# Kernel tuning notes

Hardware: AMD Instinct MI355X
Metric: run time of the kernel (lower is better)

The kernel has to match this reference:

```python
import jax, jax.numpy as jnp
import numpy as np

B, S, D = 4, 2048, 1024
H, DK, DV = 16, 64, 64


def setup_inputs() -> dict:
    key = jax.random.key(0)
    ks = jax.random.split(key, 8)
    Q = jax.random.normal(ks[0], (B, S, D), dtype=jnp.float32)
    K = jax.random.normal(ks[1], (B, S, D), dtype=jnp.float32)
    V = jax.random.normal(ks[2], (B, S, D), dtype=jnp.float32)
    attn_mask = jax.random.randint(ks[3], (B, S, S), 0, 2).astype(jnp.bool_)
    sc = 1.0 / np.sqrt(D)
    W_Q = jax.random.normal(ks[4], (D, H * DK), dtype=jnp.float32) * sc
    W_K = jax.random.normal(ks[5], (D, H * DK), dtype=jnp.float32) * sc
    W_V = jax.random.normal(ks[6], (D, H * DV), dtype=jnp.float32) * sc
    W_O = jax.random.normal(ks[7], (H * DV, D), dtype=jnp.float32) * sc
    return {"Q": Q, "K": K, "V": V, "attn_mask": attn_mask,
            "W_Q": W_Q, "W_K": W_K, "W_V": W_V, "W_O": W_O}


def reference(Q, K, V, attn_mask, W_Q, W_K, W_V, W_O):
    b = Q.shape[0]
    # project and split heads: [b, h, s, d]
    q = (Q @ W_Q).reshape(b, -1, H, DK).transpose(0, 2, 1, 3)
    k = (K @ W_K).reshape(b, -1, H, DK).transpose(0, 2, 1, 3)
    v = (V @ W_V).reshape(b, -1, H, DV).transpose(0, 2, 1, 3)
    scale = 1.0 / jnp.sqrt(jnp.asarray(DK, dtype=q.dtype))
    scores = jnp.einsum('bhsd,bhtd->bhst', q, k) * scale  # [b,h,s,s]
    scores = jnp.where(attn_mask[:, None, :, :], jnp.asarray(-1e9, dtype=scores.dtype), scores)
    attn = jax.nn.softmax(scores, axis=-1)
    ctx = jnp.einsum('bhst,bhtd->bhsd', attn, v)  # [b,h,s,dv]
    ctx = ctx.transpose(0, 2, 1, 3).reshape(b, -1, H * DV)
    return ctx @ W_O
```

## Files before the change

### kernel.cpp

```cpp
#include <hip/hip_runtime.h>
#include <stdint.h>


typedef float f32x4 __attribute__((ext_vector_type(4)));
typedef float f32x16 __attribute__((ext_vector_type(16)));
typedef __bf16 bf16x8 __attribute__((ext_vector_type(8)));
typedef int i32x2 __attribute__((ext_vector_type(2)));

__device__ __forceinline__ unsigned short f2b(float f) {
  union { float f; uint32_t u; } v; v.f = f;
  return (unsigned short)((v.u + 0x7FFFu + ((v.u >> 16) & 1u)) >> 16);
}

__device__ __forceinline__ uint32_t pkbf(float a, float b) {
  union { __bf16 h[2]; uint32_t u; } c;
  c.h[0] = (__bf16)a; c.h[1] = (__bf16)b;
  return c.u;
}

__device__ __forceinline__ float fast_exp2(float x) {
#if __has_builtin(__builtin_amdgcn_exp2f)
  return __builtin_amdgcn_exp2f(x);
#else
  return exp2f(x);
#endif
}

__device__ __forceinline__ f32x4 mfma16(bf16x8 a, bf16x8 b, f32x4 c) {
  return __builtin_amdgcn_mfma_f32_16x16x32_bf16(a, b, c, 0, 0, 0);
}

__device__ __forceinline__ f32x16 mfma32(bf16x8 a, bf16x8 b, f32x16 c) {
  return __builtin_amdgcn_mfma_f32_32x32x16_bf16(a, b, c, 0, 0, 0);
}

__device__ __forceinline__ void gld_lds16(const void* g, void* l) {
  typedef __attribute__((address_space(1))) const uint32_t GU;
  typedef __attribute__((address_space(3))) uint32_t LU;
  __builtin_amdgcn_global_load_lds((GU*)g, (LU*)l, 16, 0, 0);
}

__global__ __launch_bounds__(256) void prep_w_kernel(
    const float* __restrict__ w0, const float* __restrict__ w1,
    const float* __restrict__ w2, const float* __restrict__ w3,
    unsigned short* __restrict__ wt) {
  __shared__ float tile[64][68];
  const float* w = (blockIdx.z == 0) ? w0 : (blockIdx.z == 1) ? w1
                  : (blockIdx.z == 2) ? w2 : w3;
  unsigned short* out = wt + (size_t)blockIdx.z * (1024u * 1024u);
  const int t = threadIdx.x;
  {
    const int kr = t >> 2, cc = (t & 3) << 4;
    const float* src = w + (size_t)(blockIdx.y * 64 + kr) * 1024 + blockIdx.x * 64 + cc;
#pragma unroll
    for (int i = 0; i < 4; ++i)
      *(float4*)&tile[kr][cc + i * 4] = ((const float4*)src)[i];
  }
  __syncthreads();
  const int cl = t >> 2, kc = (t & 3) << 4;
  const int c = blockIdx.x * 64 + cl;
  union { unsigned short u[8]; uint4 q; } p0, p1;
#pragma unroll
  for (int j = 0; j < 8; ++j) {
    p0.u[j] = f2b(tile[kc + j][cl]);
    p1.u[j] = f2b(tile[kc + 8 + j][cl]);
  }
  char* rowp = (char*)out + (size_t)c * 2048;
  const uint32_t sw = (uint32_t)(c & 7) << 4;
  const uint32_t b0 = (uint32_t)(blockIdx.y * 64 + kc) * 2;
  *(uint4*)(rowp + (b0 ^ sw)) = p0.q;
  *(uint4*)(rowp + ((b0 + 16) ^ sw)) = p1.q;
}

__global__ __launch_bounds__(256) void mask_pack_kernel(
    const void* __restrict__ mask, uint32_t* __restrict__ bits) {
  __shared__ int flag;
  if (threadIdx.x == 0) flag = 0;
  __syncthreads();
  if (threadIdx.x < 64) {
    uchar4 cb = ((const uchar4*)mask)[threadIdx.x];
    if ((cb.y | cb.z | cb.w) != 0) atomicOr(&flag, 1);
  }
  __syncthreads();
  const bool is32 = (flag == 0);
  const int* ip = (const int*)mask;
  const unsigned char* bp = (const unsigned char*)mask;
  const int gw = (blockIdx.x * 256 + threadIdx.x) >> 6;
  const int lane = threadIdx.x & 63;
  const size_t base = (size_t)gw * 8192;
  for (int it = 0; it < 128; ++it) {
    size_t idx = base + (size_t)it * 64 + lane;
    int v = is32 ? ip[idx] : (int)bp[idx];
    unsigned long long m = __ballot(v != 0);
    if (lane == 0) bits[idx >> 5] = (uint32_t)m;
    if (lane == 32) bits[idx >> 5] = (uint32_t)(m >> 32);
  }
}

template <int AMODE, int OMODE>
__global__ __launch_bounds__(256) void gemm_kernel(
    const void* __restrict__ Asrc, const unsigned short* __restrict__ BT,
    void* __restrict__ Out) {
  __shared__ __align__(16) char As[128 * 128];
  __shared__ __align__(16) char Bs[128 * 128];
  const int tid = threadIdx.x;
  const int lane = tid & 63, wave = tid >> 6;
  const int g = lane >> 4, l15 = lane & 15;
  const int wm = wave >> 1, wn = wave & 1;
  const int mbase = blockIdx.x * 128, nbase = blockIdx.y * 128;

  f32x4 acc[4][4];
  const f32x4 fz = {0.f, 0.f, 0.f, 0.f};
#pragma unroll
  for (int i = 0; i < 4; ++i)
#pragma unroll
    for (int j = 0; j < 4; ++j) acc[i][j] = fz;

  for (int kb = 0; kb < 16; ++kb) {
    if (AMODE == 0) {
#pragma unroll
      for (int rr = 0; rr < 4; ++rr) {
        int row = rr * 32 + (tid >> 3);
        int kc = (tid & 7) * 8;
        const float* ap = (const float*)Asrc + (size_t)(mbase + row) * 1024 + kb * 64 + kc;
        float4 a0 = ((const float4*)ap)[0];
        float4 a1 = ((const float4*)ap)[1];
        union { __bf16 h[8]; uint4 q; } pk;
        pk.h[0] = (__bf16)a0.x; pk.h[1] = (__bf16)a0.y;
        pk.h[2] = (__bf16)a0.z; pk.h[3] = (__bf16)a0.w;
        pk.h[4] = (__bf16)a1.x; pk.h[5] = (__bf16)a1.y;
        pk.h[6] = (__bf16)a1.z; pk.h[7] = (__bf16)a1.w;
        *(uint4*)(As + row * 128 + ((kc * 2) ^ ((row & 7) << 4))) = pk.q;
      }
    } else {
      const char* ag = (const char*)Asrc + (size_t)mbase * 2048 + (size_t)kb * 128;
#pragma unroll
      for (int c = 0; c < 4; ++c) {
        int ch = wave * 4 + c;
        int row = ch * 8 + (lane >> 3);
        gld_lds16(ag + (size_t)row * 2048 + (lane & 7) * 16, As + ch * 1024);
      }
    }
    {
      const char* bg = (const char*)BT + (size_t)nbase * 2048 + (size_t)kb * 128;
#pragma unroll
      for (int c = 0; c < 4; ++c) {
        int ch = wave * 4 + c;
        int row = ch * 8 + (lane >> 3);
        gld_lds16(bg + (size_t)row * 2048 + (lane & 7) * 16, Bs + ch * 1024);
      }
    }
    __syncthreads();
#pragma unroll
    for (int kk = 0; kk < 2; ++kk) {
      bf16x8 af[4], bf[4];
#pragma unroll
      for (int mf = 0; mf < 4; ++mf) {
        int row = wm * 64 + mf * 16 + l15;
        af[mf] = *(const bf16x8*)(As + row * 128 + (((kk * 32 + g * 8) * 2) ^ ((row & 7) << 4)));
      }
#pragma unroll
      for (int nf = 0; nf < 4; ++nf) {
        int row = wn * 64 + nf * 16 + l15;
        bf[nf] = *(const bf16x8*)(Bs + row * 128 + (((kk * 32 + g * 8) * 2) ^ ((row & 7) << 4)));
      }
#pragma unroll
      for (int mf = 0; mf < 4; ++mf)
#pragma unroll
        for (int nf = 0; nf < 4; ++nf)
          acc[mf][nf] = mfma16(af[mf], bf[nf], acc[mf][nf]);
    }
    __syncthreads();
  }

  const int colbase = nbase + wn * 64 + l15;
#pragma unroll
  for (int mf = 0; mf < 4; ++mf) {
    const int grow0 = mbase + wm * 64 + mf * 16 + g * 4;
    if (OMODE == 3) {
      float* op = (float*)Out;
#pragma unroll
      for (int r = 0; r < 4; ++r)
#pragma unroll
        for (int nf = 0; nf < 4; ++nf)
          op[(size_t)(grow0 + r) * 1024 + colbase + nf * 16] = acc[mf][nf][r];
    } else if (OMODE == 0) {
      unsigned short* op = (unsigned short*)Out;
#pragma unroll
      for (int r = 0; r < 4; ++r) {
        int grow = grow0 + r, bq = grow >> 11, s = grow & 2047;
#pragma unroll
        for (int nf = 0; nf < 4; ++nf) {
          int col = colbase + nf * 16, hh = col >> 6, d = col & 63;
          op[((size_t)(bq * 16 + hh) * 2048 + s) * 64 + d] = f2b(acc[mf][nf][r]);
        }
      }
    } else if (OMODE == 1) {
      char* op = (char*)Out;
#pragma unroll
      for (int r = 0; r < 4; ++r) {
        int grow = grow0 + r, bq = grow >> 11, s = grow & 2047;
#pragma unroll
        for (int nf = 0; nf < 4; ++nf) {
          int col = colbase + nf * 16, hh = col >> 6, d = col & 63;
          *(unsigned short*)(op + ((size_t)(bq * 16 + hh) * 2048 + s) * 128 +
                             ((d * 2) ^ ((s & 7) << 4))) = f2b(acc[mf][nf][r]);
        }
      }
    } else {
      char* op = (char*)Out;
      const int bq = grow0 >> 11, s0 = grow0 & 2047;
#pragma unroll
      for (int nf = 0; nf < 4; ++nf) {
        int col = colbase + nf * 16, hh = col >> 6, d = col & 63;
        union { unsigned short u[4]; uint2 q; } pk;
#pragma unroll
        for (int r = 0; r < 4; ++r) pk.u[r] = f2b(acc[mf][nf][r]);
        *(uint2*)(op + ((size_t)(bq * 16 + hh) * 64 + d) * 4096 +
                  ((s0 * 2) ^ ((d & 7) << 4))) = pk.q;
      }
    }
  }
}

__global__ __launch_bounds__(256, 2) void attn_kernel(
    const unsigned short* __restrict__ q_ws, const char* __restrict__ k_ws,
    const char* __restrict__ vt_ws, const uint32_t* __restrict__ bits,
    char* __restrict__ ctx) {
  __shared__ __align__(16) char ks[2][8192];
  __shared__ __align__(16) char vs[2][8192];
  const int tid = threadIdx.x;
  const int lane = tid & 63, wave = tid >> 6;
  const int hi = lane >> 5, l31 = lane & 31;
  const int qt = blockIdx.x, h = blockIdx.y, b = blockIdx.z;
  const int bh = b * 16 + h;
  const int qw = qt * 128 + wave * 32;
  const char* kg = k_ws + (size_t)bh * (2048 * 128);
  const char* vg = vt_ws + (size_t)bh * (64 * 4096);

  bf16x8 bq[4];
  {
    const unsigned short* qp = q_ws + ((size_t)bh * 2048 + qw + l31) * 64 + hi * 8;
#pragma unroll
    for (int c = 0; c < 4; ++c) bq[c] = *(const bf16x8*)(qp + c * 16);
  }
  const uint32_t* mrow = bits + ((size_t)b * 2048 + qw + l31) * 64;
  uint2 mk = *(const uint2*)(mrow);

  const f32x16 fz16 = {0.f, 0.f, 0.f, 0.f, 0.f, 0.f, 0.f, 0.f,
                       0.f, 0.f, 0.f, 0.f, 0.f, 0.f, 0.f, 0.f};
  f32x16 oacc0 = fz16, oacc1 = fz16;
  float lsum = 0.f;

  const float C1 = 0.18033688011112042f;
  const float C2 = -17.312340490667562f;
  const uint32_t swl = (uint32_t)(l31 & 7) << 4;

  auto stage = [&](int t, int buf) {
    const char* kb = kg + (size_t)t * 8192;
#pragma unroll
    for (int rr = 0; rr < 2; ++rr) {
      int ch = wave * 2 + rr;
      gld_lds16(kb + ch * 1024 + lane * 16, ks[buf] + ch * 1024);
    }
    const char* vb = vg + (size_t)t * 128;
#pragma unroll
    for (int rr = 0; rr < 2; ++rr) {
      int ch = wave * 2 + rr;
      int dv = ch * 8 + (lane >> 3);
      gld_lds16(vb + (size_t)dv * 4096 + (lane & 7) * 16, vs[buf] + ch * 1024);
    }
  };

  stage(0, 0);
  __syncthreads();

  for (int tt = 0; tt < 32; ++tt) {
    const int cur = tt & 1;
    uint2 mnext = mk;
    if (tt < 31) {
      stage(tt + 1, cur ^ 1);
      mnext = *(const uint2*)(mrow + (tt + 1) * 2);
    }
    const char* kbuf = ks[cur];
    f32x16 s0 = fz16, s1 = fz16;
    __builtin_amdgcn_s_setprio(1);
#pragma unroll
    for (int c = 0; c < 4; ++c) {
      bf16x8 a0 = *(const bf16x8*)(kbuf + l31 * 128 + ((c * 32 + hi * 16) ^ swl));
      bf16x8 a1 = *(const bf16x8*)(kbuf + (32 + l31) * 128 + ((c * 32 + hi * 16) ^ swl));
      s0 = mfma32(a0, bq[c], s0);
      s1 = mfma32(a1, bq[c], s1);
    }
    __builtin_amdgcn_s_setprio(0);

    bf16x8 pa[4];
#pragma unroll
    for (int T = 0; T < 2; ++T) {
      const f32x16 sv = (T == 0) ? s0 : s1;
      const uint32_t wh = ((T == 0) ? mk.x : mk.y) >> (hi * 4);
      float e[16];
#pragma unroll
      for (int r = 0; r < 16; ++r) {
        float ex = fast_exp2(fmaf(sv[r], C1, C2));
        e[r] = ((wh >> ((r & 3) + 8 * (r >> 2))) & 1u) ? 0.f : ex;
        lsum += e[r];
      }
#pragma unroll
      for (int c2 = 0; c2 < 2; ++c2) {
        const int rb = c2 * 8;
        uint32_t x = pkbf(e[rb + 0], e[rb + 1]);
        uint32_t y = pkbf(e[rb + 2], e[rb + 3]);
        uint32_t z = pkbf(e[rb + 4], e[rb + 5]);
        uint32_t w2 = pkbf(e[rb + 6], e[rb + 7]);
        i32x2 sxz = __builtin_amdgcn_permlane32_swap((int)x, (int)z, false, false);
        i32x2 syw = __builtin_amdgcn_permlane32_swap((int)y, (int)w2, false, false);
        union { uint32_t u[4]; bf16x8 v; } fa;
        fa.u[0] = (uint32_t)sxz[0]; fa.u[1] = (uint32_t)syw[0];
        fa.u[2] = (uint32_t)sxz[1]; fa.u[3] = (uint32_t)syw[1];
        pa[T * 2 + c2] = fa.v;
      }
    }

    const char* vbuf = vs[cur];
    __builtin_amdgcn_s_setprio(1);
#pragma unroll
    for (int kc = 0; kc < 4; ++kc) {
      bf16x8 b0 = *(const bf16x8*)(vbuf + l31 * 128 + ((kc * 32 + hi * 16) ^ swl));
      bf16x8 b1 = *(const bf16x8*)(vbuf + (32 + l31) * 128 + ((kc * 32 + hi * 16) ^ swl));
      oacc0 = mfma32(pa[kc], b0, oacc0);
      oacc1 = mfma32(pa[kc], b1, oacc1);
    }
    __builtin_amdgcn_s_setprio(0);
    __syncthreads();
    mk = mnext;
  }

  lsum += __shfl_xor(lsum, 32);
  const float linv = 1.f / lsum;
  const int col0 = h * 64 + l31, col1 = col0 + 32;
#pragma unroll
  for (int r = 0; r < 16; ++r) {
    const int qloc = (r & 3) + 8 * (r >> 2) + 4 * hi;
    const float li = __shfl(linv, qloc);
    const int srow = b * 2048 + qw + qloc;
    const uint32_t swr = (uint32_t)(srow & 7) << 4;
    *(unsigned short*)(ctx + (size_t)srow * 2048 + ((col0 * 2) ^ swr)) = f2b(oacc0[r] * li);
    *(unsigned short*)(ctx + (size_t)srow * 2048 + ((col1 * 2) ^ swr)) = f2b(oacc1[r] * li);
  }
}

extern "C" void kernel_launch(void* const* d_in, const int* in_sizes, int n_in,
                              void* d_out, int out_size, void* d_ws, size_t ws_size,
                              hipStream_t stream) {
  (void)in_sizes; (void)n_in; (void)out_size; (void)ws_size;
  const float* Q = (const float*)d_in[0];
  const float* K = (const float*)d_in[1];
  const float* V = (const float*)d_in[2];
  const void* mask = d_in[3];
  const float* WQ = (const float*)d_in[4];
  const float* WK = (const float*)d_in[5];
  const float* WV = (const float*)d_in[6];
  const float* WO = (const float*)d_in[7];

  char* ws = (char*)d_ws;
  unsigned short* wt = (unsigned short*)ws;
  unsigned short* q_ws = (unsigned short*)(ws + (8ll << 20));
  char* k_ws = ws + (24ll << 20);
  char* vt_ws = ws + (40ll << 20);
  char* ctx = ws + (56ll << 20);
  uint32_t* bits = (uint32_t*)(ws + (72ll << 20));

  prep_w_kernel<<<dim3(16, 16, 4), 256, 0, stream>>>(WQ, WK, WV, WO, wt);
  mask_pack_kernel<<<dim3(512), 256, 0, stream>>>(mask, bits);
  gemm_kernel<0, 0><<<dim3(64, 8), 256, 0, stream>>>((const void*)Q, wt, (void*)q_ws);
  gemm_kernel<0, 1><<<dim3(64, 8), 256, 0, stream>>>((const void*)K, wt + (1u << 20), (void*)k_ws);
  gemm_kernel<0, 2><<<dim3(64, 8), 256, 0, stream>>>((const void*)V, wt + (2u << 20), (void*)vt_ws);
  attn_kernel<<<dim3(16, 16, 4), 256, 0, stream>>>(q_ws, k_ws, vt_ws, bits, ctx);
  gemm_kernel<1, 3><<<dim3(64, 8), 256, 0, stream>>>((const void*)ctx, wt + (3u << 20), d_out);
}
```

Baseline: 474.2 us.

## Batch QKV projections into one launch and compute softmax row sums via MFMA

Result: no change. 476.6 us (+0.5%).

```diff
diff --git a/kernel.cpp b/kernel.cpp
--- a/kernel.cpp
+++ b/kernel.cpp
@@ -97,12 +97,16 @@
   }
 }
 
-template <int AMODE, int OMODE>
-__global__ __launch_bounds__(256) void gemm_kernel(
-    const void* __restrict__ Asrc, const unsigned short* __restrict__ BT,
-    void* __restrict__ Out) {
+__global__ __launch_bounds__(256, 3) void proj_gemm_kernel(
+    const float* __restrict__ Qin, const float* __restrict__ Kin,
+    const float* __restrict__ Vin, const unsigned short* __restrict__ wt,
+    unsigned short* __restrict__ q_ws, char* __restrict__ k_ws,
+    char* __restrict__ vt_ws) {
   __shared__ __align__(16) char As[128 * 128];
   __shared__ __align__(16) char Bs[128 * 128];
+  const int z = blockIdx.z;
+  const float* Asrc = (z == 0) ? Qin : (z == 1) ? Kin : Vin;
+  const unsigned short* BT = wt + (size_t)z * (1u << 20);
   const int tid = threadIdx.x;
   const int lane = tid & 63, wave = tid >> 6;
   const int g = lane >> 4, l15 = lane & 15;
@@ -117,12 +121,12 @@
     for (int j = 0; j < 4; ++j) acc[i][j] = fz;
 
   for (int kb = 0; kb < 16; ++kb) {
-    if (AMODE == 0) {
+    {
 #pragma unroll
       for (int rr = 0; rr < 4; ++rr) {
         int row = rr * 32 + (tid >> 3);
         int kc = (tid & 7) * 8;
-        const float* ap = (const float*)Asrc + (size_t)(mbase + row) * 1024 + kb * 64 + kc;
+        const float* ap = Asrc + (size_t)(mbase + row) * 1024 + kb * 64 + kc;
         float4 a0 = ((const float4*)ap)[0];
         float4 a1 = ((const float4*)ap)[1];
         union { __bf16 h[8]; uint4 q; } pk;
@@ -132,14 +136,6 @@
         pk.h[6] = (__bf16)a1.z; pk.h[7] = (__bf16)a1.w;
         *(uint4*)(As + row * 128 + ((kc * 2) ^ ((row & 7) << 4))) = pk.q;
       }
-    } else {
-      const char* ag = (const char*)Asrc + (size_t)mbase * 2048 + (size_t)kb * 128;
-#pragma unroll
-      for (int c = 0; c < 4; ++c) {
-        int ch = wave * 4 + c;
-        int row = ch * 8 + (lane >> 3);
-        gld_lds16(ag + (size_t)row * 2048 + (lane & 7) * 16, As + ch * 1024);
-      }
     }
     {
       const char* bg = (const char*)BT + (size_t)nbase * 2048 + (size_t)kb * 128;
@@ -177,15 +173,8 @@
 #pragma unroll
   for (int mf = 0; mf < 4; ++mf) {
     const int grow0 = mbase + wm * 64 + mf * 16 + g * 4;
-    if (OMODE == 3) {
-      float* op = (float*)Out;
-#pragma unroll
-      for (int r = 0; r < 4; ++r)
-#pragma unroll
-        for (int nf = 0; nf < 4; ++nf)
-          op[(size_t)(grow0 + r) * 1024 + colbase + nf * 16] = acc[mf][nf][r];
-    } else if (OMODE == 0) {
-      unsigned short* op = (unsigned short*)Out;
+    if (z == 0) {
+      unsigned short* op = q_ws;
 #pragma unroll
       for (int r = 0; r < 4; ++r) {
         int grow = grow0 + r, bq = grow >> 11, s = grow & 2047;
@@ -195,8 +184,8 @@
           op[((size_t)(bq * 16 + hh) * 2048 + s) * 64 + d] = f2b(acc[mf][nf][r]);
         }
       }
-    } else if (OMODE == 1) {
-      char* op = (char*)Out;
+    } else if (z == 1) {
+      char* op = k_ws;
 #pragma unroll
       for (int r = 0; r < 4; ++r) {
         int grow = grow0 + r, bq = grow >> 11, s = grow & 2047;
@@ -208,7 +197,7 @@
         }
       }
     } else {
-      char* op = (char*)Out;
+      char* op = vt_ws;
       const int bq = grow0 >> 11, s0 = grow0 & 2047;
 #pragma unroll
       for (int nf = 0; nf < 4; ++nf) {
@@ -223,7 +212,79 @@
   }
 }
 
-__global__ __launch_bounds__(256, 2) void attn_kernel(
+__global__ __launch_bounds__(256) void out_gemm_kernel(
+    const char* __restrict__ Asrc, const unsigned short* __restrict__ BT,
+    float* __restrict__ Out) {
+  __shared__ __align__(16) char As[128 * 128];
+  __shared__ __align__(16) char Bs[128 * 128];
+  const int tid = threadIdx.x;
+  const int lane = tid & 63, wave = tid >> 6;
+  const int g = lane >> 4, l15 = lane & 15;
+  const int wm = wave >> 1, wn = wave & 1;
+  const int mbase = blockIdx.x * 128, nbase = blockIdx.y * 128;
+
+  f32x4 acc[4][4];
+  const f32x4 fz = {0.f, 0.f, 0.f, 0.f};
+#pragma unroll
+  for (int i = 0; i < 4; ++i)
+#pragma unroll
+    for (int j = 0; j < 4; ++j) acc[i][j] = fz;
+
+  for (int kb = 0; kb < 16; ++kb) {
+    {
+      const char* ag = Asrc + (size_t)mbase * 2048 + (size_t)kb * 128;
+#pragma unroll
+      for (int c = 0; c < 4; ++c) {
+        int ch = wave * 4 + c;
+        int row = ch * 8 + (lane >> 3);
+        gld_lds16(ag + (size_t)row * 2048 + (lane & 7) * 16, As + ch * 1024);
+      }
+    }
+    {
+      const char* bg = (const char*)BT + (size_t)nbase * 2048 + (size_t)kb * 128;
+#pragma unroll
+      for (int c = 0; c < 4; ++c) {
+        int ch = wave * 4 + c;
+        int row = ch * 8 + (lane >> 3);
+        gld_lds16(bg + (size_t)row * 2048 + (lane & 7) * 16, Bs + ch * 1024);
+      }
+    }
+    __syncthreads();
+#pragma unroll
+    for (int kk = 0; kk < 2; ++kk) {
+      bf16x8 af[4], bf[4];
+#pragma unroll
+      for (int mf = 0; mf < 4; ++mf) {
+        int row = wm * 64 + mf * 16 + l15;
+        af[mf] = *(const bf16x8*)(As + row * 128 + (((kk * 32 + g * 8) * 2) ^ ((row & 7) << 4)));
+      }
+#pragma unroll
+      for (int nf = 0; nf < 4; ++nf) {
+        int row = wn * 64 + nf * 16 + l15;
+        bf[nf] = *(const bf16x8*)(Bs + row * 128 + (((kk * 32 + g * 8) * 2) ^ ((row & 7) << 4)));
+      }
+#pragma unroll
+      for (int mf = 0; mf < 4; ++mf)
+#pragma unroll
+        for (int nf = 0; nf < 4; ++nf)
+          acc[mf][nf] = mfma16(af[mf], bf[nf], acc[mf][nf]);
+    }
+    __syncthreads();
+  }
+
+  const int colbase = nbase + wn * 64 + l15;
+#pragma unroll
+  for (int mf = 0; mf < 4; ++mf) {
+    const int grow0 = mbase + wm * 64 + mf * 16 + g * 4;
+#pragma unroll
+    for (int r = 0; r < 4; ++r)
+#pragma unroll
+      for (int nf = 0; nf < 4; ++nf)
+        Out[(size_t)(grow0 + r) * 1024 + colbase + nf * 16] = acc[mf][nf][r];
+  }
+}
+
+__global__ __launch_bounds__(256, 4) void attn_kernel(
     const unsigned short* __restrict__ q_ws, const char* __restrict__ k_ws,
     const char* __restrict__ vt_ws, const uint32_t* __restrict__ bits,
     char* __restrict__ ctx) {
@@ -249,8 +310,12 @@
 
   const f32x16 fz16 = {0.f, 0.f, 0.f, 0.f, 0.f, 0.f, 0.f, 0.f,
                        0.f, 0.f, 0.f, 0.f, 0.f, 0.f, 0.f, 0.f};
-  f32x16 oacc0 = fz16, oacc1 = fz16;
-  float lsum = 0.f;
+  f32x16 oacc0 = fz16, oacc1 = fz16, sacc = fz16;
+
+  union { unsigned short u[8]; bf16x8 v; } onesu;
+#pragma unroll
+  for (int i = 0; i < 8; ++i) onesu.u[i] = 0x3F80;
+  const bf16x8 ones = onesu.v;
 
   const float C1 = 0.18033688011112042f;
   const float C2 = -17.312340490667562f;
@@ -304,7 +369,6 @@
       for (int r = 0; r < 16; ++r) {
         float ex = fast_exp2(fmaf(sv[r], C1, C2));
         e[r] = ((wh >> ((r & 3) + 8 * (r >> 2))) & 1u) ? 0.f : ex;
-        lsum += e[r];
       }
 #pragma unroll
       for (int c2 = 0; c2 < 2; ++c2) {
@@ -330,19 +394,18 @@
       bf16x8 b1 = *(const bf16x8*)(vbuf + (32 + l31) * 128 + ((kc * 32 + hi * 16) ^ swl));
       oacc0 = mfma32(pa[kc], b0, oacc0);
       oacc1 = mfma32(pa[kc], b1, oacc1);
+      sacc = mfma32(pa[kc], ones, sacc);
     }
     __builtin_amdgcn_s_setprio(0);
     __syncthreads();
     mk = mnext;
   }
 
-  lsum += __shfl_xor(lsum, 32);
-  const float linv = 1.f / lsum;
   const int col0 = h * 64 + l31, col1 = col0 + 32;
 #pragma unroll
   for (int r = 0; r < 16; ++r) {
     const int qloc = (r & 3) + 8 * (r >> 2) + 4 * hi;
-    const float li = __shfl(linv, qloc);
+    const float li = 1.f / sacc[r];
     const int srow = b * 2048 + qw + qloc;
     const uint32_t swr = (uint32_t)(srow & 7) << 4;
     *(unsigned short*)(ctx + (size_t)srow * 2048 + ((col0 * 2) ^ swr)) = f2b(oacc0[r] * li);
@@ -373,9 +436,7 @@
 
   prep_w_kernel<<<dim3(16, 16, 4), 256, 0, stream>>>(WQ, WK, WV, WO, wt);
   mask_pack_kernel<<<dim3(512), 256, 0, stream>>>(mask, bits);
-  gemm_kernel<0, 0><<<dim3(64, 8), 256, 0, stream>>>((const void*)Q, wt, (void*)q_ws);
-  gemm_kernel<0, 1><<<dim3(64, 8), 256, 0, stream>>>((const void*)K, wt + (1u << 20), (void*)k_ws);
-  gemm_kernel<0, 2><<<dim3(64, 8), 256, 0, stream>>>((const void*)V, wt + (2u << 20), (void*)vt_ws);
+  proj_gemm_kernel<<<dim3(64, 8, 3), 256, 0, stream>>>(Q, K, V, wt, q_ws, k_ws, vt_ws);
   attn_kernel<<<dim3(16, 16, 4), 256, 0, stream>>>(q_ws, k_ws, vt_ws, bits, ctx);
-  gemm_kernel<1, 3><<<dim3(64, 8), 256, 0, stream>>>((const void*)ctx, wt + (3u << 20), d_out);
-}
+  out_gemm_kernel<<<dim3(64, 8), 256, 0, stream>>>(ctx, wt + (3u << 20), (float*)d_out);
+}
```
